# Performance work log

Measured on AMD Instinct MI355X. Metric: run time of the kernel, lower is better.

The kernel has to match this reference:

```python
import jax, jax.numpy as jnp
import numpy as np

B, S, HID = 4, 2048, 576
NH, NKV, HD = 9, 3, 64
MAXPOS, THETA = 8192, 100000.0


def rotate_half(x):
    x1, x2 = x[..., : x.shape[-1] // 2], x[..., x.shape[-1] // 2 :]
    return jnp.concatenate((-x2, x1), axis=-1)


def setup_inputs() -> dict:
    key = jax.random.key(0)
    ks = jax.random.split(key, 6)
    x = jax.random.normal(ks[0], (B, S, HID), dtype=jnp.float32)
    # RoPE tables (HuggingFace layout: freqs duplicated across halves)
    inv_freq = 1.0 / (THETA ** (np.arange(0, HD, 2, dtype=np.float32) / HD))
    freqs = np.outer(np.arange(MAXPOS, dtype=np.float32), inv_freq)
    emb = np.concatenate([freqs, freqs], axis=-1)
    cos = jnp.asarray(np.cos(emb))
    sin = jnp.asarray(np.sin(emb))
    position_ids = jnp.broadcast_to(jnp.arange(S, dtype=jnp.int64), (B, S))
    # additive causal mask [B,1,S,S]
    causal = jnp.where(
        jnp.tril(jnp.ones((S, S), dtype=bool)), 0.0, -1e9
    ).astype(jnp.float32)
    attention_mask = jnp.broadcast_to(causal, (B, 1, S, S))
    scale = 0.02
    wq = jax.random.normal(ks[1], (NH * HD, HID), dtype=jnp.float32) * scale
    wk = jax.random.normal(ks[2], (NKV * HD, HID), dtype=jnp.float32) * scale
    wv = jax.random.normal(ks[3], (NKV * HD, HID), dtype=jnp.float32) * scale
    wo = jax.random.normal(ks[4], (HID, NH * HD), dtype=jnp.float32) * scale
    return {
        "x": x, "cos": cos, "sin": sin, "position_ids": position_ids,
        "attention_mask": attention_mask,
        "wq": wq, "wk": wk, "wv": wv, "wo": wo,
    }


def reference(x, cos, sin, position_ids, attention_mask, wq, wk, wv, wo):
    b, s, _ = x.shape
    # projections (nn.Linear: y = x @ W.T), split into heads -> [B,H,S,D]
    q = (x @ wq.T).reshape(b, s, NH, HD).transpose(0, 2, 1, 3)
    k = (x @ wk.T).reshape(b, s, NKV, HD).transpose(0, 2, 1, 3)
    v = (x @ wv.T).reshape(b, s, NKV, HD).transpose(0, 2, 1, 3)
    # RoPE: cos/sin gathered per position -> [B,1,S,D], broadcast over heads
    c = cos[position_ids][:, None, :, :]
    si = sin[position_ids][:, None, :, :]
    q = q * c + rotate_half(q) * si
    k = k * c + rotate_half(k) * si
    # GQA expansion: repeat_interleave kv heads to match q heads
    k = jnp.repeat(k, NH // NKV, axis=1)
    v = jnp.repeat(v, NH // NKV, axis=1)
    scale = 1.0 / jnp.sqrt(jnp.asarray(HD, dtype=x.dtype))
    scores = jnp.einsum("bhqd,bhkd->bhqk", q, k) * scale + attention_mask
    attn = jax.nn.softmax(scores.astype(jnp.float32), axis=-1).astype(q.dtype)
    out = jnp.einsum("bhqk,bhkd->bhqd", attn, v)
    out = out.transpose(0, 2, 1, 3).reshape(b, s, NH * HD)
    return out @ wo.T
```

## Files before the change

kernel.cpp:

```cpp
#include <hip/hip_runtime.h>
#include <hip/hip_bf16.h>

#define B_    4
#define S_    2048
#define HID_  576
#define NH_   9
#define NKV_  3
#define HD_   64
#define GQ_   3

typedef __attribute__((ext_vector_type(8))) short bf16x8;
typedef __attribute__((ext_vector_type(4))) float f32x4;

__device__ __forceinline__ short f2bf(float f) {
    union { float f; unsigned int u; } v; v.f = f;
    unsigned int r = (v.u + 0x7fffu + ((v.u >> 16) & 1u)) >> 16;
    return (short)r;
}

__device__ __forceinline__ void async16(const void* g, void* l) {
    __builtin_amdgcn_global_load_lds(
        (const __attribute__((address_space(1))) unsigned int*)g,
        (__attribute__((address_space(3))) unsigned int*)l, 16, 0, 0);
}

#define NX_   (8192 * 576)
#define NWQ_  (576 * 576)
#define NWK_  (192 * 576)
#define NWV_  (192 * 576)
#define NWO_  (576 * 576)
#define NTOT_ (NX_ + NWQ_ + NWK_ + NWV_ + NWO_)

__global__ __launch_bounds__(256) void convert_kernel(
    const float* __restrict__ x,  const float* __restrict__ wq,
    const float* __restrict__ wk, const float* __restrict__ wv,
    const float* __restrict__ wo,
    short* __restrict__ xb, short* __restrict__ wqkvb, short* __restrict__ wob)
{
    int i4 = (blockIdx.x * 256 + threadIdx.x) * 4;
    const float* src; short* dst;
    if (i4 < NX_)                          { src = x  + i4;                          dst = xb    + i4; }
    else if (i4 < NX_ + NWQ_)              { src = wq + (i4 - NX_);                  dst = wqkvb + (i4 - NX_); }
    else if (i4 < NX_ + NWQ_ + NWK_)       { src = wk + (i4 - NX_ - NWQ_);           dst = wqkvb + (i4 - NX_); }
    else if (i4 < NX_ + NWQ_ + NWK_ + NWV_){ src = wv + (i4 - NX_ - NWQ_ - NWK_);    dst = wqkvb + (i4 - NX_); }
    else                                   { src = wo + (i4 - NX_ - NWQ_ - NWK_ - NWV_);
                                             dst = wob + (i4 - NX_ - NWQ_ - NWK_ - NWV_); }
    float4 v = *(const float4*)src;
    short4 o = make_short4(f2bf(v.x), f2bf(v.y), f2bf(v.z), f2bf(v.w));
    *(short4*)dst = o;
}

__global__ __launch_bounds__(256) void qkv_kernel(
    const short* __restrict__ xb,
    const short* __restrict__ wqkvb,
    const float* __restrict__ cosb,
    const float* __restrict__ sinb,
    short* __restrict__ Q,
    short* __restrict__ K,
    short* __restrict__ Vt)
{
    __shared__ __align__(16) short As[128 * 64];
    __shared__ __align__(16) short Bs[64 * 64];

    const int m0     = blockIdx.x * 128;
    const int nb_blk = blockIdx.y;
    const int tid  = threadIdx.x;
    const int w    = tid >> 6, lane = tid & 63;
    const int quad = lane >> 4, c = lane & 15;
    const int lr   = lane >> 3, lg = lane & 7;
    const int sw   = lg ^ lr;
    const int xg   = quad ^ (c & 7);

    f32x4 acc[2][4];
    #pragma unroll
    for (int mf = 0; mf < 2; ++mf)
        #pragma unroll
        for (int nb = 0; nb < 4; ++nb) acc[mf][nb] = (f32x4){0.f, 0.f, 0.f, 0.f};

    for (int kk = 0; kk < 9; ++kk) {
        const int k0 = kk * 64;
        __syncthreads();
        #pragma unroll
        for (int r = 0; r < 4; ++r) {
            int ch = w * 4 + r;
            int R  = ch * 8 + lr;
            async16(xb + (size_t)(m0 + R) * HID_ + k0 + sw * 8,
                    (char*)As + ch * 1024);
        }
        #pragma unroll
        for (int r = 0; r < 2; ++r) {
            int ch = w * 2 + r;
            int R  = ch * 8 + lr;
            async16(wqkvb + (size_t)(nb_blk * 64 + R) * HID_ + k0 + sw * 8,
                    (char*)Bs + ch * 1024);
        }
        __syncthreads();

        bf16x8 a[2][2], bfr[4][2];
        #pragma unroll
        for (int mf = 0; mf < 2; ++mf) {
            int row = w * 32 + mf * 16 + c;
            a[mf][0] = *(const bf16x8*)(As + row * 64 + xg * 8);
            a[mf][1] = *(const bf16x8*)(As + row * 64 + (xg ^ 4) * 8);
        }
        #pragma unroll
        for (int nb = 0; nb < 4; ++nb) {
            int row = nb * 16 + c;
            bfr[nb][0] = *(const bf16x8*)(Bs + row * 64 + xg * 8);
            bfr[nb][1] = *(const bf16x8*)(Bs + row * 64 + (xg ^ 4) * 8);
        }
        #pragma unroll
        for (int mf = 0; mf < 2; ++mf)
            #pragma unroll
            for (int nb = 0; nb < 4; ++nb) {
                acc[mf][nb] = __builtin_amdgcn_mfma_f32_16x16x32_bf16(a[mf][0], bfr[nb][0], acc[mf][nb], 0, 0, 0);
                acc[mf][nb] = __builtin_amdgcn_mfma_f32_16x16x32_bf16(a[mf][1], bfr[nb][1], acc[mf][nb], 0, 0, 0);
            }
    }

    int type, head;
    if (nb_blk < NH_)            { type = 0; head = nb_blk; }
    else if (nb_blk < NH_ + NKV_){ type = 1; head = nb_blk - NH_; }
    else                         { type = 2; head = nb_blk - NH_ - NKV_; }
    const int b  = m0 >> 11;
    const int s0 = m0 & (S_ - 1);

    if (type < 2) {
        #pragma unroll
        for (int mf = 0; mf < 2; ++mf)
            #pragma unroll
            for (int reg = 0; reg < 4; ++reg) {
                int s = s0 + w * 32 + mf * 16 + quad * 4 + reg;
                const float* cr = cosb + (size_t)s * HD_;
                const float* sr = sinb + (size_t)s * HD_;
                float a0 = acc[mf][0][reg], a1 = acc[mf][1][reg];
                float a2 = acc[mf][2][reg], a3 = acc[mf][3][reg];
                float o0 = a0 * cr[c]      - a2 * sr[c];
                float o1 = a1 * cr[c + 16] - a3 * sr[c + 16];
                float o2 = a2 * cr[c + 32] + a0 * sr[c + 32];
                float o3 = a3 * cr[c + 48] + a1 * sr[c + 48];
                short* dst = (type == 0)
                    ? Q + (((size_t)b * NH_  + head) * S_ + s) * HD_
                    : K + (((size_t)b * NKV_ + head) * S_ + s) * HD_;
                dst[c]      = f2bf(o0);
                dst[c + 16] = f2bf(o1);
                dst[c + 32] = f2bf(o2);
                dst[c + 48] = f2bf(o3);
            }
    } else {
        short* base = Vt + (((size_t)b * NKV_ + head) * HD_) * S_;
        #pragma unroll
        for (int mf = 0; mf < 2; ++mf) {
            int s4 = s0 + w * 32 + mf * 16 + quad * 4;
            #pragma unroll
            for (int nb = 0; nb < 4; ++nb) {
                int d = nb * 16 + c;
                short4 pk = make_short4(f2bf(acc[mf][nb][0]), f2bf(acc[mf][nb][1]),
                                        f2bf(acc[mf][nb][2]), f2bf(acc[mf][nb][3]));
                *(short4*)(base + (size_t)d * S_ + s4) = pk;
            }
        }
    }
}

__global__ __launch_bounds__(256) void attn_kernel(
    const short* __restrict__ Q,
    const short* __restrict__ K,
    const short* __restrict__ Vt,
    short* __restrict__ AOb)
{
    __shared__ __align__(16) short Qs[64 * 64];
    __shared__ __align__(16) short Ks[2][64 * 64];
    __shared__ __align__(16) short Vs[2][64 * 64];
    __shared__ __align__(16) short Ps[64][72];

    const int hb = blockIdx.x;
    const int h  = hb >> 2, b = hb & 3;
    const int qt = 31 - blockIdx.y;
    const int kh = h / GQ_;
    const int tid  = threadIdx.x;
    const int w    = tid >> 6, lane = tid & 63;
    const int quad = lane >> 4, c = lane & 15;
    const int lr   = lane >> 3, lg = lane & 7;
    const int sw   = lg ^ lr;
    const int xg   = quad ^ (c & 7);

    const short* Qg = Q  + (((size_t)b * NH_  + h ) * S_ + qt * 64) * HD_;
    const short* Kg = K  + (((size_t)b * NKV_ + kh) * S_) * HD_;
    const short* Vg = Vt + (((size_t)b * NKV_ + kh) * HD_) * S_;

    #pragma unroll
    for (int r = 0; r < 2; ++r) {
        int ch = w * 2 + r;
        int R  = ch * 8 + lr;
        async16(Qg + (size_t)R * HD_ + sw * 8, (char*)Qs + ch * 1024);
    }
    #pragma unroll
    for (int r = 0; r < 4; ++r) {
        int it = w * 4 + r;
        if (it < 8) {
            int R = it * 8 + lr;
            async16(Kg + (size_t)R * HD_ + sw * 8, (char*)Ks[0] + it * 1024);
        } else {
            int R = (it - 8) * 8 + lr;
            async16(Vg + (size_t)R * S_ + sw * 8, (char*)Vs[0] + (it - 8) * 1024);
        }
    }

    f32x4 acc_o[4];
    #pragma unroll
    for (int nb = 0; nb < 4; ++nb) acc_o[nb] = (f32x4){0.f, 0.f, 0.f, 0.f};
    float mrow[4], lrow[4];
    #pragma unroll
    for (int r = 0; r < 4; ++r) { mrow[r] = -1e30f; lrow[r] = 0.f; }

    const float scale = 0.125f;
    int buf = 0;

    for (int kt = 0; kt <= qt; ++kt) {
        __syncthreads();
        if (kt < qt) {
            int nxt = buf ^ 1;
            #pragma unroll
            for (int r = 0; r < 4; ++r) {
                int it = w * 4 + r;
                if (it < 8) {
                    int R = it * 8 + lr;
                    async16(Kg + (size_t)((kt + 1) * 64 + R) * HD_ + sw * 8,
                            (char*)Ks[nxt] + it * 1024);
                } else {
                    int R = (it - 8) * 8 + lr;
                    async16(Vg + (size_t)R * S_ + (kt + 1) * 64 + sw * 8,
                            (char*)Vs[nxt] + (it - 8) * 1024);
                }
            }
        }
        const short* ks = Ks[buf];
        const short* vs = Vs[buf];

        bf16x8 aq0 = *(const bf16x8*)(Qs + (w * 16 + c) * 64 + xg * 8);
        bf16x8 aq1 = *(const bf16x8*)(Qs + (w * 16 + c) * 64 + (xg ^ 4) * 8);
        f32x4 sc[4];
        #pragma unroll
        for (int nb = 0; nb < 4; ++nb) {
            bf16x8 bk0 = *(const bf16x8*)(ks + (nb * 16 + c) * 64 + xg * 8);
            bf16x8 bk1 = *(const bf16x8*)(ks + (nb * 16 + c) * 64 + (xg ^ 4) * 8);
            f32x4 z = (f32x4){0.f, 0.f, 0.f, 0.f};
            z = __builtin_amdgcn_mfma_f32_16x16x32_bf16(aq0, bk0, z, 0, 0, 0);
            z = __builtin_amdgcn_mfma_f32_16x16x32_bf16(aq1, bk1, z, 0, 0, 0);
            sc[nb] = z;
        }

        const bool diag = (kt == qt);
        #pragma unroll
        for (int r = 0; r < 4; ++r) {
            const int qrow = w * 16 + quad * 4 + r;
            float v[4];
            float rmax = -1e30f;
            #pragma unroll
            for (int nb = 0; nb < 4; ++nb) {
                float sv = sc[nb][r] * scale;
                if (diag && (nb * 16 + c > qrow)) sv = -1e30f;
                v[nb] = sv;
                rmax = fmaxf(rmax, sv);
            }
            rmax = fmaxf(rmax, __shfl_xor(rmax, 1));
            rmax = fmaxf(rmax, __shfl_xor(rmax, 2));
            rmax = fmaxf(rmax, __shfl_xor(rmax, 4));
            rmax = fmaxf(rmax, __shfl_xor(rmax, 8));
            float mnew  = fmaxf(mrow[r], rmax);
            float alpha = __expf(mrow[r] - mnew);
            mrow[r] = mnew;
            float rsum = 0.f;
            #pragma unroll
            for (int nb = 0; nb < 4; ++nb) {
                float p = __expf(v[nb] - mnew);
                rsum += p;
                Ps[w * 16 + quad * 4 + r][nb * 16 + c] = f2bf(p);
            }
            rsum += __shfl_xor(rsum, 1);
            rsum += __shfl_xor(rsum, 2);
            rsum += __shfl_xor(rsum, 4);
            rsum += __shfl_xor(rsum, 8);
            lrow[r] = lrow[r] * alpha + rsum;
            #pragma unroll
            for (int nb = 0; nb < 4; ++nb) acc_o[nb][r] *= alpha;
        }

        #pragma unroll
        for (int kc = 0; kc < 2; ++kc) {
            bf16x8 ap = *(const bf16x8*)&Ps[w * 16 + c][quad * 8 + kc * 32];
            int pg = kc ? (xg ^ 4) : xg;
            #pragma unroll
            for (int nb = 0; nb < 4; ++nb) {
                bf16x8 bv = *(const bf16x8*)(vs + (nb * 16 + c) * 64 + pg * 8);
                acc_o[nb] = __builtin_amdgcn_mfma_f32_16x16x32_bf16(ap, bv, acc_o[nb], 0, 0, 0);
            }
        }
        buf ^= 1;
    }

    #pragma unroll
    for (int r = 0; r < 4; ++r) {
        int s = qt * 64 + w * 16 + quad * 4 + r;
        float inv = 1.f / lrow[r];
        short* dst = AOb + (((size_t)b * S_ + s) * NH_ + h) * HD_;
        #pragma unroll
        for (int nb = 0; nb < 4; ++nb)
            dst[nb * 16 + c] = f2bf(acc_o[nb][r] * inv);
    }
}

__global__ __launch_bounds__(256) void oproj_kernel(
    const short* __restrict__ AOb,
    const short* __restrict__ wob,
    float* __restrict__ out)
{
    __shared__ __align__(16) short As[128 * 64];
    __shared__ __align__(16) short Bs[64 * 64];

    const int m0 = blockIdx.x * 128;
    const int n0 = blockIdx.y * 64;
    const int tid  = threadIdx.x;
    const int w    = tid >> 6, lane = tid & 63;
    const int quad = lane >> 4, c = lane & 15;
    const int lr   = lane >> 3, lg = lane & 7;
    const int sw   = lg ^ lr;
    const int xg   = quad ^ (c & 7);

    f32x4 acc[2][4];
    #pragma unroll
    for (int mf = 0; mf < 2; ++mf)
        #pragma unroll
        for (int nb = 0; nb < 4; ++nb) acc[mf][nb] = (f32x4){0.f, 0.f, 0.f, 0.f};

    for (int kk = 0; kk < 9; ++kk) {
        const int k0 = kk * 64;
        __syncthreads();
        #pragma unroll
        for (int r = 0; r < 4; ++r) {
            int ch = w * 4 + r;
            int R  = ch * 8 + lr;
            async16(AOb + (size_t)(m0 + R) * HID_ + k0 + sw * 8,
                    (char*)As + ch * 1024);
        }
        #pragma unroll
        for (int r = 0; r < 2; ++r) {
            int ch = w * 2 + r;
            int R  = ch * 8 + lr;
            async16(wob + (size_t)(n0 + R) * HID_ + k0 + sw * 8,
                    (char*)Bs + ch * 1024);
        }
        __syncthreads();

        bf16x8 a[2][2], bfr[4][2];
        #pragma unroll
        for (int mf = 0; mf < 2; ++mf) {
            int row = w * 32 + mf * 16 + c;
            a[mf][0] = *(const bf16x8*)(As + row * 64 + xg * 8);
            a[mf][1] = *(const bf16x8*)(As + row * 64 + (xg ^ 4) * 8);
        }
        #pragma unroll
        for (int nb = 0; nb < 4; ++nb) {
            int row = nb * 16 + c;
            bfr[nb][0] = *(const bf16x8*)(Bs + row * 64 + xg * 8);
            bfr[nb][1] = *(const bf16x8*)(Bs + row * 64 + (xg ^ 4) * 8);
        }
        #pragma unroll
        for (int mf = 0; mf < 2; ++mf)
            #pragma unroll
            for (int nb = 0; nb < 4; ++nb) {
                acc[mf][nb] = __builtin_amdgcn_mfma_f32_16x16x32_bf16(a[mf][0], bfr[nb][0], acc[mf][nb], 0, 0, 0);
                acc[mf][nb] = __builtin_amdgcn_mfma_f32_16x16x32_bf16(a[mf][1], bfr[nb][1], acc[mf][nb], 0, 0, 0);
            }
    }

    #pragma unroll
    for (int mf = 0; mf < 2; ++mf)
        #pragma unroll
        for (int reg = 0; reg < 4; ++reg) {
            int m = m0 + w * 32 + mf * 16 + quad * 4 + reg;
            float* dst = out + (size_t)m * HID_ + n0;
            #pragma unroll
            for (int nb = 0; nb < 4; ++nb)
                dst[nb * 16 + c] = acc[mf][nb][reg];
        }
}

extern "C" void kernel_launch(void* const* d_in, const int* in_sizes, int n_in,
                              void* d_out, int out_size, void* d_ws, size_t ws_size,
                              hipStream_t stream) {
    const float* x    = (const float*)d_in[0];
    const float* cosb = (const float*)d_in[1];
    const float* sinb = (const float*)d_in[2];
    const float* wq   = (const float*)d_in[5];
    const float* wk   = (const float*)d_in[6];
    const float* wv   = (const float*)d_in[7];
    const float* wo   = (const float*)d_in[8];

    short* xb    = (short*)d_ws;
    short* wqkvb = xb    + (size_t)NX_;
    short* wob   = wqkvb + (size_t)(NWQ_ + NWK_ + NWV_);
    short* Qb    = wob   + (size_t)NWO_;
    short* Kb    = Qb    + (size_t)B_ * NH_  * S_ * HD_;
    short* Vtb   = Kb    + (size_t)B_ * NKV_ * S_ * HD_;
    short* AOb   = Vtb   + (size_t)B_ * NKV_ * S_ * HD_;

    convert_kernel<<<dim3(NTOT_ / 4 / 256), dim3(256), 0, stream>>>(
        x, wq, wk, wv, wo, xb, wqkvb, wob);
    qkv_kernel<<<dim3(64, 15), dim3(256), 0, stream>>>(
        xb, wqkvb, cosb, sinb, Qb, Kb, Vtb);
    attn_kernel<<<dim3(36, 32), dim3(256), 0, stream>>>(Qb, Kb, Vtb, AOb);
    oproj_kernel<<<dim3(64, 9), dim3(256), 0, stream>>>(AOb, wob, (float*)d_out);
}
```

Measured before the change: 215.0 us.

## Triple-buffer GEMM loads, fold softmax scale into Q, MFMA row sums

```diff
diff --git a/kernel.cpp b/kernel.cpp
--- a/kernel.cpp
+++ b/kernel.cpp
@@ -59,8 +59,8 @@
     short* __restrict__ K,
     short* __restrict__ Vt)
 {
-    __shared__ __align__(16) short As[128 * 64];
-    __shared__ __align__(16) short Bs[64 * 64];
+    __shared__ __align__(16) short As[3][128 * 64];
+    __shared__ __align__(16) short Bs[3][64 * 64];
 
     const int m0     = blockIdx.x * 128;
     const int nb_blk = blockIdx.y;
@@ -71,43 +71,49 @@
     const int sw   = lg ^ lr;
     const int xg   = quad ^ (c & 7);
 
+    auto stage = [&](int step, short* dstA, short* dstB) {
+        const int k0 = step * 64;
+        #pragma unroll
+        for (int r = 0; r < 4; ++r) {
+            int ch = w * 4 + r, R = ch * 8 + lr;
+            async16(xb + (size_t)(m0 + R) * HID_ + k0 + sw * 8, (char*)dstA + ch * 1024);
+        }
+        #pragma unroll
+        for (int r = 0; r < 2; ++r) {
+            int ch = w * 2 + r, R = ch * 8 + lr;
+            async16(wqkvb + (size_t)(nb_blk * 64 + R) * HID_ + k0 + sw * 8, (char*)dstB + ch * 1024);
+        }
+    };
+
     f32x4 acc[2][4];
     #pragma unroll
     for (int mf = 0; mf < 2; ++mf)
         #pragma unroll
         for (int nb = 0; nb < 4; ++nb) acc[mf][nb] = (f32x4){0.f, 0.f, 0.f, 0.f};
 
+    stage(0, As[0], Bs[0]);
+    stage(1, As[1], Bs[1]);
+
     for (int kk = 0; kk < 9; ++kk) {
-        const int k0 = kk * 64;
-        __syncthreads();
-        #pragma unroll
-        for (int r = 0; r < 4; ++r) {
-            int ch = w * 4 + r;
-            int R  = ch * 8 + lr;
-            async16(xb + (size_t)(m0 + R) * HID_ + k0 + sw * 8,
-                    (char*)As + ch * 1024);
-        }
-        #pragma unroll
-        for (int r = 0; r < 2; ++r) {
-            int ch = w * 2 + r;
-            int R  = ch * 8 + lr;
-            async16(wqkvb + (size_t)(nb_blk * 64 + R) * HID_ + k0 + sw * 8,
-                    (char*)Bs + ch * 1024);
-        }
-        __syncthreads();
-
+        if (kk < 8) __builtin_amdgcn_s_waitcnt(0x0F76);
+        else        __builtin_amdgcn_s_waitcnt(0x0F70);
+        __builtin_amdgcn_s_barrier();
+        if (kk + 2 < 9) stage(kk + 2, As[(kk + 2) % 3], Bs[(kk + 2) % 3]);
+
+        const short* a_s = As[kk % 3];
+        const short* b_s = Bs[kk % 3];
         bf16x8 a[2][2], bfr[4][2];
         #pragma unroll
         for (int mf = 0; mf < 2; ++mf) {
             int row = w * 32 + mf * 16 + c;
-            a[mf][0] = *(const bf16x8*)(As + row * 64 + xg * 8);
-            a[mf][1] = *(const bf16x8*)(As + row * 64 + (xg ^ 4) * 8);
+            a[mf][0] = *(const bf16x8*)(a_s + row * 64 + xg * 8);
+            a[mf][1] = *(const bf16x8*)(a_s + row * 64 + (xg ^ 4) * 8);
         }
         #pragma unroll
         for (int nb = 0; nb < 4; ++nb) {
             int row = nb * 16 + c;
-            bfr[nb][0] = *(const bf16x8*)(Bs + row * 64 + xg * 8);
-            bfr[nb][1] = *(const bf16x8*)(Bs + row * 64 + (xg ^ 4) * 8);
+            bfr[nb][0] = *(const bf16x8*)(b_s + row * 64 + xg * 8);
+            bfr[nb][1] = *(const bf16x8*)(b_s + row * 64 + (xg ^ 4) * 8);
         }
         #pragma unroll
         for (int mf = 0; mf < 2; ++mf)
@@ -126,6 +132,7 @@
     const int s0 = m0 & (S_ - 1);
 
     if (type < 2) {
+        const float qs = (type == 0) ? 0.125f : 1.0f;
         #pragma unroll
         for (int mf = 0; mf < 2; ++mf)
             #pragma unroll
@@ -135,10 +142,10 @@
                 const float* sr = sinb + (size_t)s * HD_;
                 float a0 = acc[mf][0][reg], a1 = acc[mf][1][reg];
                 float a2 = acc[mf][2][reg], a3 = acc[mf][3][reg];
-                float o0 = a0 * cr[c]      - a2 * sr[c];
-                float o1 = a1 * cr[c + 16] - a3 * sr[c + 16];
-                float o2 = a2 * cr[c + 32] + a0 * sr[c + 32];
-                float o3 = a3 * cr[c + 48] + a1 * sr[c + 48];
+                float o0 = (a0 * cr[c]      - a2 * sr[c])      * qs;
+                float o1 = (a1 * cr[c + 16] - a3 * sr[c + 16]) * qs;
+                float o2 = (a2 * cr[c + 32] + a0 * sr[c + 32]) * qs;
+                float o3 = (a3 * cr[c + 48] + a1 * sr[c + 48]) * qs;
                 short* dst = (type == 0)
                     ? Q + (((size_t)b * NH_  + head) * S_ + s) * HD_
                     : K + (((size_t)b * NKV_ + head) * S_ + s) * HD_;
@@ -162,6 +169,8 @@
         }
     }
 }
+
+#define PSTR 72
 
 __global__ __launch_bounds__(256) void attn_kernel(
     const short* __restrict__ Q,
@@ -172,7 +181,7 @@
     __shared__ __align__(16) short Qs[64 * 64];
     __shared__ __align__(16) short Ks[2][64 * 64];
     __shared__ __align__(16) short Vs[2][64 * 64];
-    __shared__ __align__(16) short Ps[64][72];
+    __shared__ __align__(16) short Ps[64 * PSTR];
 
     const int hb = blockIdx.x;
     const int h  = hb >> 2, b = hb & 3;
@@ -191,8 +200,7 @@
 
     #pragma unroll
     for (int r = 0; r < 2; ++r) {
-        int ch = w * 2 + r;
-        int R  = ch * 8 + lr;
+        int ch = w * 2 + r, R = ch * 8 + lr;
         async16(Qg + (size_t)R * HD_ + sw * 8, (char*)Qs + ch * 1024);
     }
     #pragma unroll
@@ -207,18 +215,27 @@
         }
     }
 
+    bf16x8 ones;
+    #pragma unroll
+    for (int i = 0; i < 8; ++i) ones[i] = (short)0x3F80;
+
+    bf16x8 aq0, aq1;
     f32x4 acc_o[4];
     #pragma unroll
     for (int nb = 0; nb < 4; ++nb) acc_o[nb] = (f32x4){0.f, 0.f, 0.f, 0.f};
-    float mrow[4], lrow[4];
-    #pragma unroll
-    for (int r = 0; r < 4; ++r) { mrow[r] = -1e30f; lrow[r] = 0.f; }
-
-    const float scale = 0.125f;
+    f32x4 acc_l = (f32x4){0.f, 0.f, 0.f, 0.f};
+    float mrow[4];
+    #pragma unroll
+    for (int r = 0; r < 4; ++r) mrow[r] = -1e30f;
+
     int buf = 0;
 
     for (int kt = 0; kt <= qt; ++kt) {
         __syncthreads();
+        if (kt == 0) {
+            aq0 = *(const bf16x8*)(Qs + (w * 16 + c) * 64 + xg * 8);
+            aq1 = *(const bf16x8*)(Qs + (w * 16 + c) * 64 + (xg ^ 4) * 8);
+        }
         if (kt < qt) {
             int nxt = buf ^ 1;
             #pragma unroll
@@ -238,8 +255,6 @@
         const short* ks = Ks[buf];
         const short* vs = Vs[buf];
 
-        bf16x8 aq0 = *(const bf16x8*)(Qs + (w * 16 + c) * 64 + xg * 8);
-        bf16x8 aq1 = *(const bf16x8*)(Qs + (w * 16 + c) * 64 + (xg ^ 4) * 8);
         f32x4 sc[4];
         #pragma unroll
         for (int nb = 0; nb < 4; ++nb) {
@@ -259,7 +274,7 @@
             float rmax = -1e30f;
             #pragma unroll
             for (int nb = 0; nb < 4; ++nb) {
-                float sv = sc[nb][r] * scale;
+                float sv = sc[nb][r];
                 if (diag && (nb * 16 + c > qrow)) sv = -1e30f;
                 v[nb] = sv;
                 rmax = fmaxf(rmax, sv);
@@ -271,31 +286,24 @@
             float mnew  = fmaxf(mrow[r], rmax);
             float alpha = __expf(mrow[r] - mnew);
             mrow[r] = mnew;
-            float rsum = 0.f;
-            #pragma unroll
-            for (int nb = 0; nb < 4; ++nb) {
-                float p = __expf(v[nb] - mnew);
-                rsum += p;
-                Ps[w * 16 + quad * 4 + r][nb * 16 + c] = f2bf(p);
-            }
-            rsum += __shfl_xor(rsum, 1);
-            rsum += __shfl_xor(rsum, 2);
-            rsum += __shfl_xor(rsum, 4);
-            rsum += __shfl_xor(rsum, 8);
-            lrow[r] = lrow[r] * alpha + rsum;
+            #pragma unroll
+            for (int nb = 0; nb < 4; ++nb)
+                Ps[(w * 16 + quad * 4 + r) * PSTR + nb * 16 + c] = f2bf(__expf(v[nb] - mnew));
             #pragma unroll
             for (int nb = 0; nb < 4; ++nb) acc_o[nb][r] *= alpha;
+            acc_l[r] *= alpha;
         }
 
         #pragma unroll
         for (int kc = 0; kc < 2; ++kc) {
-            bf16x8 ap = *(const bf16x8*)&Ps[w * 16 + c][quad * 8 + kc * 32];
+            bf16x8 ap = *(const bf16x8*)(Ps + (w * 16 + c) * PSTR + quad * 8 + kc * 32);
             int pg = kc ? (xg ^ 4) : xg;
             #pragma unroll
             for (int nb = 0; nb < 4; ++nb) {
                 bf16x8 bv = *(const bf16x8*)(vs + (nb * 16 + c) * 64 + pg * 8);
                 acc_o[nb] = __builtin_amdgcn_mfma_f32_16x16x32_bf16(ap, bv, acc_o[nb], 0, 0, 0);
             }
+            acc_l = __builtin_amdgcn_mfma_f32_16x16x32_bf16(ap, ones, acc_l, 0, 0, 0);
         }
         buf ^= 1;
     }
@@ -303,7 +311,7 @@
     #pragma unroll
     for (int r = 0; r < 4; ++r) {
         int s = qt * 64 + w * 16 + quad * 4 + r;
-        float inv = 1.f / lrow[r];
+        float inv = 1.f / acc_l[r];
         short* dst = AOb + (((size_t)b * S_ + s) * NH_ + h) * HD_;
         #pragma unroll
         for (int nb = 0; nb < 4; ++nb)
@@ -316,8 +324,8 @@
     const short* __restrict__ wob,
     float* __restrict__ out)
 {
-    __shared__ __align__(16) short As[128 * 64];
-    __shared__ __align__(16) short Bs[64 * 64];
+    __shared__ __align__(16) short As[3][128 * 64];
+    __shared__ __align__(16) short Bs[3][64 * 64];
 
     const int m0 = blockIdx.x * 128;
     const int n0 = blockIdx.y * 64;
@@ -328,43 +336,49 @@
     const int sw   = lg ^ lr;
     const int xg   = quad ^ (c & 7);
 
+    auto stage = [&](int step, short* dstA, short* dstB) {
+        const int k0 = step * 64;
+        #pragma unroll
+        for (int r = 0; r < 4; ++r) {
+            int ch = w * 4 + r, R = ch * 8 + lr;
+            async16(AOb + (size_t)(m0 + R) * HID_ + k0 + sw * 8, (char*)dstA + ch * 1024);
+        }
+        #pragma unroll
+        for (int r = 0; r < 2; ++r) {
+            int ch = w * 2 + r, R = ch * 8 + lr;
+            async16(wob + (size_t)(n0 + R) * HID_ + k0 + sw * 8, (char*)dstB + ch * 1024);
+        }
+    };
+
     f32x4 acc[2][4];
     #pragma unroll
     for (int mf = 0; mf < 2; ++mf)
         #pragma unroll
         for (int nb = 0; nb < 4; ++nb) acc[mf][nb] = (f32x4){0.f, 0.f, 0.f, 0.f};
 
+    stage(0, As[0], Bs[0]);
+    stage(1, As[1], Bs[1]);
+
     for (int kk = 0; kk < 9; ++kk) {
-        const int k0 = kk * 64;
-        __syncthreads();
-        #pragma unroll
-        for (int r = 0; r < 4; ++r) {
-            int ch = w * 4 + r;
-            int R  = ch * 8 + lr;
-            async16(AOb + (size_t)(m0 + R) * HID_ + k0 + sw * 8,
-                    (char*)As + ch * 1024);
-        }
-        #pragma unroll
-        for (int r = 0; r < 2; ++r) {
-            int ch = w * 2 + r;
-            int R  = ch * 8 + lr;
-            async16(wob + (size_t)(n0 + R) * HID_ + k0 + sw * 8,
-                    (char*)Bs + ch * 1024);
-        }
-        __syncthreads();
-
+        if (kk < 8) __builtin_amdgcn_s_waitcnt(0x0F76);
+        else        __builtin_amdgcn_s_waitcnt(0x0F70);
+        __builtin_amdgcn_s_barrier();
+        if (kk + 2 < 9) stage(kk + 2, As[(kk + 2) % 3], Bs[(kk + 2) % 3]);
+
+        const short* a_s = As[kk % 3];
+        const short* b_s = Bs[kk % 3];
         bf16x8 a[2][2], bfr[4][2];
         #pragma unroll
         for (int mf = 0; mf < 2; ++mf) {
             int row = w * 32 + mf * 16 + c;
-            a[mf][0] = *(const bf16x8*)(As + row * 64 + xg * 8);
-            a[mf][1] = *(const bf16x8*)(As + row * 64 + (xg ^ 4) * 8);
+            a[mf][0] = *(const bf16x8*)(a_s + row * 64 + xg * 8);
+            a[mf][1] = *(const bf16x8*)(a_s + row * 64 + (xg ^ 4) * 8);
         }
         #pragma unroll
         for (int nb = 0; nb < 4; ++nb) {
             int row = nb * 16 + c;
-            bfr[nb][0] = *(const bf16x8*)(Bs + row * 64 + xg * 8);
-            bfr[nb][1] = *(const bf16x8*)(Bs + row * 64 + (xg ^ 4) * 8);
+            bfr[nb][0] = *(const bf16x8*)(b_s + row * 64 + xg * 8);
+            bfr[nb][1] = *(const bf16x8*)(b_s + row * 64 + (xg ^ 4) * 8);
         }
         #pragma unroll
         for (int mf = 0; mf < 2; ++mf)
```

Result: no change. 213.9 us (-0.5%).
